# Kernel tuning notes

Measured on AMD Instinct MI355X. Metric: run time of the kernel, lower is better.

The kernel has to match this reference:

```python
import jax, jax.numpy as jnp
import numpy as np

THETA = 0.7
KS = 3          # deformable-conv kernel size
N = KS * KS     # 9 sampling points


def setup_inputs() -> dict:
    key = jax.random.key(0)
    k = jax.random.split(key, 7)
    B, C, H, W = 2, 256, 64, 64
    x = jax.random.normal(k[0], (B, C, H, W), jnp.float32)
    # offset-predicting conv (3x3, pad 1), 2*N output channels; small init so offsets are sane
    p_w = jax.random.normal(k[1], (2 * N, C, 3, 3), jnp.float32) * 0.01
    p_b = jax.random.normal(k[2], (2 * N,), jnp.float32) * 0.01
    # modulation conv (3x3, pad 1), N output channels
    m_w = jax.random.normal(k[3], (N, C, 3, 3), jnp.float32) * 0.01
    m_b = jnp.zeros((N,), jnp.float32)
    # final deform conv weight (applied as ks x ks, stride ks over the unfolded map), no bias
    dconv_w = jax.random.normal(k[4], (256, C, KS, KS), jnp.float32) * 0.05
    # central-difference conv raw weight, shape (Cout, Cin, 1, 5), no bias
    cdc_w = jax.random.normal(k[5], (256, C, 1, 5), jnp.float32) * 0.05
    return {"x": x, "p_w": p_w, "p_b": p_b, "m_w": m_w, "m_b": m_b,
            "dconv_w": dconv_w, "cdc_w": cdc_w}


def _conv2d(x, w, pad):
    return jax.lax.conv_general_dilated(
        x, w, window_strides=(1, 1), padding=pad,
        dimension_numbers=("NCHW", "OIHW", "NCHW"))


def deform_conv(x, p_w, p_b, m_w, m_b, dconv_w):
    B, C, H, W = x.shape
    same = [(1, 1), (1, 1)]
    offset = _conv2d(x, p_w, same) + p_b[None, :, None, None]          # [B,2N,H,W]
    m = jax.nn.sigmoid(_conv2d(x, m_w, same) + m_b[None, :, None, None])  # [B,N,H,W]

    xp = jnp.pad(x, ((0, 0), (0, 0), (1, 1), (1, 1)))  # zero padding 1
    Hp, Wp = H + 2, W + 2

    # p = p_0 + p_n + offset  (x = row coord, y = col coord; torch meshgrid 'ij')
    p_n_x = jnp.repeat(jnp.arange(-1, 2, dtype=x.dtype), 3)   # [-1,-1,-1,0,0,0,1,1,1]
    p_n_y = jnp.tile(jnp.arange(-1, 2, dtype=x.dtype), 3)     # [-1,0,1,-1,0,1,-1,0,1]
    rows = jnp.arange(1, H + 1, dtype=x.dtype)                # p_0_x
    cols = jnp.arange(1, W + 1, dtype=x.dtype)                # p_0_y
    px = offset[:, :N] + p_n_x[None, :, None, None] + rows[None, None, :, None]
    py = offset[:, N:] + p_n_y[None, :, None, None] + cols[None, None, None, :]
    px = jnp.transpose(px, (0, 2, 3, 1))  # [B,H,W,N]
    py = jnp.transpose(py, (0, 2, 3, 1))

    # integer corners from UNCLAMPED p (detached), as in the original
    fx = jnp.floor(jax.lax.stop_gradient(px))
    fy = jnp.floor(jax.lax.stop_gradient(py))
    qx0 = jnp.clip(fx, 0, Hp - 1)
    qy0 = jnp.clip(fy, 0, Wp - 1)
    qx1 = jnp.clip(fx + 1, 0, Hp - 1)
    qy1 = jnp.clip(fy + 1, 0, Wp - 1)

    # clamp p before computing bilinear weights (original order)
    pxc = jnp.clip(px, 0, Hp - 1)
    pyc = jnp.clip(py, 0, Wp - 1)
    g_lt = (1 + (qx0 - pxc)) * (1 + (qy0 - pyc))
    g_rb = (1 - (qx1 - pxc)) * (1 - (qy1 - pyc))
    g_lb = (1 + (qx0 - pxc)) * (1 - (qy1 - pyc))
    g_rt = (1 - (qx1 - pxc)) * (1 + (qy0 - pyc))

    xf = xp.reshape(B, C, Hp * Wp)

    def gather(qx, qy):
        idx = (qx.astype(jnp.int32) * Wp + qy.astype(jnp.int32)).reshape(B, 1, -1)
        return jnp.take_along_axis(xf, idx, axis=2).reshape(B, C, H, W, N)

    x_off = (g_lt[:, None] * gather(qx0, qy0)
             + g_rb[:, None] * gather(qx1, qy1)
             + g_lb[:, None] * gather(qx0, qy1)
             + g_rt[:, None] * gather(qx1, qy0))          # [B,C,H,W,N]
    x_off = x_off * jnp.transpose(m, (0, 2, 3, 1))[:, None]  # modulation broadcast over C

    # conv(ksxks, stride ks) over the unfolded map == contraction over the N taps;
    # tap n = 3r + c corresponds to kernel position (r, c)
    w = dconv_w.reshape(dconv_w.shape[0], C, N)
    return jnp.einsum("bchwn,ocn->bohw", x_off, w)


def cdc_conv(x, cdc_w):
    Co, Ci = cdc_w.shape[0], cdc_w.shape[1]
    z = jnp.zeros((Co, Ci, 1), cdc_w.dtype)
    wk = jnp.concatenate(
        [z, cdc_w[:, :, :, 0], z, cdc_w[:, :, :, 1], cdc_w[:, :, :, 2],
         cdc_w[:, :, :, 3], z, cdc_w[:, :, :, 4], z], axis=2
    ).reshape(Co, Ci, 3, 3)
    out_normal = _conv2d(x, wk, [(1, 1), (1, 1)])
    kdiff = cdc_w.sum(axis=(2, 3))[:, :, None, None]
    out_diff = _conv2d(x, kdiff, [(0, 0), (0, 0)])
    return out_normal - THETA * out_diff


def reference(x, p_w, p_b, m_w, m_b, dconv_w, cdc_w):
    out_dc = jax.nn.relu(deform_conv(x, p_w, p_b, m_w, m_b, dconv_w))
    out_cdc = jax.nn.relu(cdc_conv(x, cdc_w))
    return jnp.concatenate([out_dc, out_cdc], axis=1)  # [B,512,H,W]
```

## Files before the change

kernel.cpp:

```cpp
#include <hip/hip_runtime.h>
#include <hip/hip_bf16.h>
#include <math.h>

#define XT_BSTRIDE (66*66*256)
#define THETA_ 0.7f

typedef unsigned short u16;
typedef __attribute__((ext_vector_type(8))) short bf16x8;
typedef __attribute__((ext_vector_type(4))) float f32x4;

#define GLOAD16(gp, lp) __builtin_amdgcn_global_load_lds( \
    (const __attribute__((address_space(1))) unsigned int*)(gp), \
    (__attribute__((address_space(3))) unsigned int*)(lp), 16, 0, 0)

#define WAIT_VMCNT(N) asm volatile("s_waitcnt vmcnt(" #N ")" ::: "memory")

__device__ __forceinline__ void bar_fenced() {
  __builtin_amdgcn_sched_barrier(0);
  __builtin_amdgcn_s_barrier();
  __builtin_amdgcn_sched_barrier(0);
}

__device__ __forceinline__ float bf2f(u16 v) {
  union { unsigned u; float f; } x; x.u = ((unsigned)v) << 16; return x.f;
}
__device__ __forceinline__ u16 f2bf(float f) {
  __hip_bfloat16 h = __float2bfloat16(f);
  return *(u16*)&h;
}

__device__ __forceinline__ size_t swz_idx(int row, int k, int KT) {
  int kt = k >> 6, kc = (k >> 3) & 7, kj = k & 7;
  return (size_t)row * KT + kt * 64 + ((kc ^ (row & 7)) << 3) + kj;
}

__global__ __launch_bounds__(256) void prep(
    const float* __restrict__ x, const float* __restrict__ p_w,
    const float* __restrict__ m_w, const float* __restrict__ dconv_w,
    const float* __restrict__ cdc_w, u16* __restrict__ xTb,
    u16* __restrict__ W1t, u16* __restrict__ Wdt, u16* __restrict__ Wct) {
  int blk = blockIdx.x;
  if (blk < 512) {
    int cg = blk & 3;
    int h  = (blk >> 2) & 63;
    int b  = blk >> 8;
    __shared__ float tile[64][65];
    const float* xp = x + ((size_t)(b * 256 + cg * 64)) * 4096 + h * 64;
#pragma unroll
    for (int j = 0; j < 16; j++) {
      int idx = j * 256 + threadIdx.x;
      int ci = idx >> 6, w = idx & 63;
      tile[ci][w] = xp[(size_t)ci * 4096 + w];
    }
    __syncthreads();
    u16* xo = xTb + (size_t)b * XT_BSTRIDE + ((h + 1) * 66 + 1) * 256 + cg * 64;
#pragma unroll
    for (int j = 0; j < 16; j++) {
      int idx = j * 256 + threadIdx.x;
      int w = idx >> 6, ci = idx & 63;
      xo[(size_t)w * 256 + ci] = f2bf(tile[ci][w]);
    }
    return;
  }
  if (blk < 1032) {
    int i = (blk - 512) * 256 + threadIdx.x;
    if (i >= 133120) return;
    int c = i & 255;
    int j = i >> 8;
    int b = (j >= 260) ? 1 : 0;
    int r = j - b * 260;
    int hp, wp;
    if (r < 66)       { hp = 0;        wp = r; }
    else if (r < 132) { hp = 65;       wp = r - 66; }
    else if (r < 196) { hp = r - 131;  wp = 0; }
    else              { hp = r - 195;  wp = 65; }
    xTb[(size_t)b * XT_BSTRIDE + (hp * 66 + wp) * 256 + c] = 0;
    return;
  }
  int i = (blk - 1032) * 256 + threadIdx.x;
  if (i < 73728) {
    int o = i / 2304, k = i % 2304;
    int kp = k >> 8, c = k & 255;
    float v = 0.f;
    if (o < 18)      v = p_w[((size_t)o * 256 + c) * 9 + kp];
    else if (o < 27) v = m_w[((size_t)(o - 18) * 256 + c) * 9 + kp];
    W1t[swz_idx(o, k, 2304)] = f2bf(v);
    return;
  }
  int j = i - 73728;
  if (j < 589824) {
    int o = j / 2304, k = j % 2304;
    int n = k >> 8, c = k & 255;
    Wdt[swz_idx(o, k, 2304)] = f2bf(dconv_w[((size_t)o * 256 + c) * 9 + n]);
    return;
  }
  int j2 = j - 589824;
  if (j2 < 327680) {
    int o = j2 / 1280, k = j2 % 1280;
    int t = k >> 8, c = k & 255;
    const float* cw = cdc_w + ((size_t)o * 256 + c) * 5;
    float v = cw[t];
    if (t == 2) v -= THETA_ * (cw[0] + cw[1] + cw[2] + cw[3] + cw[4]);
    Wct[swz_idx(o, k, 1280)] = f2bf(v);
  }
}

__global__ __launch_bounds__(256) void gather_Ad(const u16* __restrict__ xTb,
                                                 const float* __restrict__ omp,
                                                 const float* __restrict__ p_b,
                                                 const float* __restrict__ m_b,
                                                 u16* __restrict__ Ad) {
  int gid = blockIdx.x * 256 + threadIdx.x;
  int q = gid & 31;
  int s = gid >> 5;
  int p = s / 9, n = s - p * 9;
  int b = p >> 12;
  int hw = p & 4095;
  int h = hw >> 6, w = hw & 63;

  float offx = p_b[n], offy = p_b[9 + n], mraw = m_b[n];
#pragma unroll
  for (int ks = 0; ks < 4; ks++) {
    const float* base = omp + ks * 221184 + b * 110592;
    offx += base[(size_t)n * 4096 + hw];
    offy += base[(size_t)(9 + n) * 4096 + hw];
    mraw += base[(size_t)(18 + n) * 4096 + hw];
  }
  float px = offx + (float)(h + n / 3);
  float py = offy + (float)(w + n % 3);
  float fx = floorf(px), fy = floorf(py);
  float qx0 = fminf(fmaxf(fx, 0.f), 65.f);
  float qy0 = fminf(fmaxf(fy, 0.f), 65.f);
  float qx1 = fminf(fmaxf(fx + 1.f, 0.f), 65.f);
  float qy1 = fminf(fmaxf(fy + 1.f, 0.f), 65.f);
  float pxc = fminf(fmaxf(px, 0.f), 65.f);
  float pyc = fminf(fmaxf(py, 0.f), 65.f);
  float gx0 = 1.f + (qx0 - pxc);
  float gx1 = 1.f - (qx1 - pxc);
  float gy0 = 1.f + (qy0 - pyc);
  float gy1 = 1.f - (qy1 - pyc);
  float m = 1.f / (1.f + expf(-mraw));
  int i0 = (int)qx0 * 66 + (int)qy0;
  int i1 = (int)qx1 * 66 + (int)qy1;
  int i2 = (int)qx0 * 66 + (int)qy1;
  int i3 = (int)qx1 * 66 + (int)qy0;
  float g0 = gx0 * gy0 * m, g1 = gx1 * gy1 * m;
  float g2 = gx0 * gy1 * m, g3 = gx1 * gy0 * m;

  const u16* xb = xTb + (size_t)b * XT_BSTRIDE + q * 8;
  bf16x8 a0 = *(const bf16x8*)(xb + (size_t)i0 * 256);
  bf16x8 a1 = *(const bf16x8*)(xb + (size_t)i1 * 256);
  bf16x8 a2 = *(const bf16x8*)(xb + (size_t)i2 * 256);
  bf16x8 a3 = *(const bf16x8*)(xb + (size_t)i3 * 256);
  bf16x8 ov;
#pragma unroll
  for (int j = 0; j < 8; j++) {
    float v = g0 * bf2f((u16)a0[j]) + g1 * bf2f((u16)a1[j]) +
              g2 * bf2f((u16)a2[j]) + g3 * bf2f((u16)a3[j]);
    ov[j] = (short)f2bf(v);
  }
  int k = n * 256 + q * 8;
  int kt = k >> 6, kc = (k >> 3) & 7;
  *(bf16x8*)(Ad + (size_t)p * 2304 + kt * 64 + (((kc ^ (p & 7)) << 3))) = ov;
}

template <int KTOT, int MODE>
__device__ __forceinline__ void gemm_body(
    const u16* __restrict__ Asrc, const u16* __restrict__ Bt,
    float* __restrict__ outp, int mt, int nt, u16* As, u16* Bs) {
  const int NKT = KTOT / 64;
  const int OCH0 = (MODE == 1) ? 256 : 0;
  int tid = threadIdx.x;
  int wid = tid >> 6, lane = tid & 63;
  int wr = wid >> 1, wc = wid & 1;
  int pbase = mt * 64;
  int obase = nt * 64;
  int l8 = lane >> 3, l7 = lane & 7;
  int lr = lane & 15, lg = lane >> 4;

  f32x4 acc[2][2];
#pragma unroll
  for (int i = 0; i < 2; i++)
#pragma unroll
    for (int j = 0; j < 2; j++) acc[i][j] = {0.f, 0.f, 0.f, 0.f};

  const int dh1[5] = {0, 1, 1, 1, 2}, dw1[5] = {1, 0, 1, 2, 1};

  auto stage = [&](int kt, u16* Ah, u16* Bh) {
    if (MODE == 0) {
#pragma unroll
      for (int i = 0; i < 2; i++) {
        int r0 = wid * 16 + i * 8;
        const u16* g = Asrc + (size_t)(pbase + r0 + l8) * KTOT + kt * 64 + (l7 << 3);
        GLOAD16(g, &Ah[r0 * 64]);
      }
    } else {
      int t = kt >> 2, c0 = (kt & 3) << 6;
      int dh = dh1[t], dw = dw1[t];
#pragma unroll
      for (int i = 0; i < 2; i++) {
        int r0 = wid * 16 + i * 8;
        int r = r0 + l8;
        int p = pbase + r;
        int b = p >> 12, hw = p & 4095, h = hw >> 6, w = hw & 63;
        int chunk = l7 ^ (r & 7);
        const u16* g = Asrc + (size_t)b * XT_BSTRIDE +
                       ((h + dh) * 66 + (w + dw)) * 256 + c0 + (chunk << 3);
        GLOAD16(g, &Ah[r0 * 64]);
      }
    }
#pragma unroll
    for (int i = 0; i < 2; i++) {
      int o0 = wid * 16 + i * 8;
      const u16* g = Bt + (size_t)(obase + o0 + l8) * KTOT + kt * 64 + (l7 << 3);
      GLOAD16(g, &Bh[o0 * 64]);
    }
  };

  stage(0, As, Bs);

  for (int it = 0; it < NKT; it++) {
    int cur = it & 1;
    u16* Ac = As + cur * 4096;
    u16* Bc = Bs + cur * 4096;

    bar_fenced();
    if (it + 1 < NKT) {
      stage(it + 1, As + (cur ^ 1) * 4096, Bs + (cur ^ 1) * 4096);
      WAIT_VMCNT(4);
    } else {
      WAIT_VMCNT(0);
    }
    bar_fenced();

    bf16x8 av[2][2], bv[2][2];
#pragma unroll
    for (int mf = 0; mf < 2; mf++) {
      int r = wr * 32 + mf * 16 + lr;
#pragma unroll
      for (int ks = 0; ks < 2; ks++) {
        int kc = ks * 4 + lg;
        av[mf][ks] = *(const bf16x8*)&Ac[r * 64 + ((kc ^ (r & 7)) << 3)];
      }
    }
#pragma unroll
    for (int nf = 0; nf < 2; nf++) {
      int o = wc * 32 + nf * 16 + lr;
#pragma unroll
      for (int ks = 0; ks < 2; ks++) {
        int kc = ks * 4 + lg;
        bv[nf][ks] = *(const bf16x8*)&Bc[o * 64 + ((kc ^ (o & 7)) << 3)];
      }
    }
#pragma unroll
    for (int nf = 0; nf < 2; nf++)
#pragma unroll
      for (int mf = 0; mf < 2; mf++)
#pragma unroll
        for (int ks = 0; ks < 2; ks++)
          acc[nf][mf] = __builtin_amdgcn_mfma_f32_16x16x32_bf16(
              bv[nf][ks], av[mf][ks], acc[nf][mf], 0, 0, 0);
  }

#pragma unroll
  for (int nf = 0; nf < 2; nf++)
#pragma unroll
    for (int mf = 0; mf < 2; mf++) {
      int p = pbase + wr * 32 + mf * 16 + lr;
      int hw = p & 4095, b = p >> 12;
      int og = OCH0 + obase + wc * 32 + nf * 16 + lg * 4;
      f32x4 v = acc[nf][mf];
#pragma unroll
      for (int e = 0; e < 4; e++)
        outp[(size_t)(b * 512 + og + e) * 4096 + hw] = fmaxf(v[e], 0.f);
    }
}

__device__ __forceinline__ void offmod_body(
    const u16* __restrict__ xTb, const u16* __restrict__ Bt,
    float* __restrict__ outp, int mt, int kt0, int nkt, u16* As, u16* Bs) {
  int tid = threadIdx.x;
  int wid = tid >> 6, lane = tid & 63;
  int pbase = mt * 128;
  int l8 = lane >> 3, l7 = lane & 7;
  int lr = lane & 15, lg = lane >> 4;

  f32x4 acc[2][2];
#pragma unroll
  for (int i = 0; i < 2; i++)
#pragma unroll
    for (int j = 0; j < 2; j++) acc[i][j] = {0.f, 0.f, 0.f, 0.f};

  auto stage = [&](int kt, u16* Ah, u16* Bh) {
    int t = kt >> 2, c0 = (kt & 3) << 6;
    int dh = t / 3, dw = t % 3;
#pragma unroll
    for (int i = 0; i < 4; i++) {
      int r0 = wid * 32 + i * 8;
      int r = r0 + l8;
      int p = pbase + r;
      int b = p >> 12, hw = p & 4095, h = hw >> 6, w = hw & 63;
      int chunk = l7 ^ (r & 7);
      const u16* g = xTb + (size_t)b * XT_BSTRIDE +
                     ((h + dh) * 66 + (w + dw)) * 256 + c0 + (chunk << 3);
      GLOAD16(g, &Ah[r0 * 64]);
    }
    {
      int o0 = wid * 8;
      const u16* g = Bt + (size_t)(o0 + l8) * 2304 + kt * 64 + (l7 << 3);
      GLOAD16(g, &Bh[o0 * 64]);
    }
  };

  stage(kt0, As, Bs);

  for (int it = 0; it < nkt; it++) {
    int cur = it & 1;
    u16* Ac = As + cur * 8192;
    u16* Bc = Bs + cur * 2048;

    bar_fenced();
    if (it + 1 < nkt) {
      stage(kt0 + it + 1, As + (cur ^ 1) * 8192, Bs + (cur ^ 1) * 2048);
      WAIT_VMCNT(5);
    } else {
      WAIT_VMCNT(0);
    }
    bar_fenced();

    bf16x8 av[2][2], bv[2][2];
#pragma unroll
    for (int mf = 0; mf < 2; mf++) {
      int r = wid * 32 + mf * 16 + lr;
#pragma unroll
      for (int ks = 0; ks < 2; ks++) {
        int kc = ks * 4 + lg;
        av[mf][ks] = *(const bf16x8*)&Ac[r * 64 + ((kc ^ (r & 7)) << 3)];
      }
    }
#pragma unroll
    for (int nf = 0; nf < 2; nf++) {
      int o = nf * 16 + lr;
#pragma unroll
      for (int ks = 0; ks < 2; ks++) {
        int kc = ks * 4 + lg;
        bv[nf][ks] = *(const bf16x8*)&Bc[o * 64 + ((kc ^ (o & 7)) << 3)];
      }
    }
#pragma unroll
    for (int nf = 0; nf < 2; nf++)
#pragma unroll
      for (int mf = 0; mf < 2; mf++)
#pragma unroll
        for (int ks = 0; ks < 2; ks++)
          acc[nf][mf] = __builtin_amdgcn_mfma_f32_16x16x32_bf16(
              bv[nf][ks], av[mf][ks], acc[nf][mf], 0, 0, 0);
  }

#pragma unroll
  for (int nf = 0; nf < 2; nf++)
#pragma unroll
    for (int mf = 0; mf < 2; mf++) {
      int p = pbase + wid * 32 + mf * 16 + lr;
      int hw = p & 4095, b = p >> 12;
      int o0 = nf * 16 + lg * 4;
      f32x4 v = acc[nf][mf];
#pragma unroll
      for (int e = 0; e < 4; e++) {
        int o = o0 + e;
        if (o < 27)
          outp[(size_t)(b * 27 + o) * 4096 + hw] = v[e];
      }
    }
}

__global__ __launch_bounds__(256) void gemm_offmod(const u16* __restrict__ xTb,
                                                   const u16* __restrict__ W1t,
                                                   float* __restrict__ omp) {
  __shared__ u16 As[2 * 128 * 64];
  __shared__ u16 Bs[2 * 32 * 64];
  int bid = blockIdx.x;
  int xcd = bid & 7;
  int i = bid >> 3;
  int mt = xcd * 8 + (i & 7);
  int ks = i >> 3;
  offmod_body(xTb, W1t, omp + ks * 221184, mt, ks * 9, 9, As, Bs);
}

__global__ __launch_bounds__(256, 4) void gemm_main(const u16* __restrict__ Ad,
                                                    const u16* __restrict__ xTb,
                                                    const u16* __restrict__ Wdt,
                                                    const u16* __restrict__ Wct,
                                                    float* __restrict__ out) {
  __shared__ u16 As[2 * 64 * 64];
  __shared__ u16 Bs[2 * 64 * 64];
  int bid = blockIdx.x;
  int fam = bid & 1;
  int idx = bid >> 1;
  int xcd = idx & 7;
  int j = idx >> 3;
  int mt = xcd * 16 + (j & 15);
  int nt = j >> 4;
  if (fam == 0) gemm_body<2304, 0>(Ad, Wdt, out, mt, nt, As, Bs);
  else          gemm_body<1280, 1>(xTb, Wct, out, mt, nt, As, Bs);
}

extern "C" void kernel_launch(void* const* d_in, const int* in_sizes, int n_in,
                              void* d_out, int out_size, void* d_ws, size_t ws_size,
                              hipStream_t stream) {
  (void)in_sizes; (void)n_in; (void)out_size; (void)ws_size;
  const float* x       = (const float*)d_in[0];
  const float* p_w     = (const float*)d_in[1];
  const float* p_b     = (const float*)d_in[2];
  const float* m_w     = (const float*)d_in[3];
  const float* m_b     = (const float*)d_in[4];
  const float* dconv_w = (const float*)d_in[5];
  const float* cdc_w   = (const float*)d_in[6];
  float* out = (float*)d_out;
  char* ws = (char*)d_ws;

  u16*   xTb  = (u16*)(ws);
  float* omp  = (float*)(ws + 4460544);
  u16*   W1t  = (u16*)(ws + 7999488);
  u16*   Wdt  = (u16*)(ws + 8146944);
  u16*   Wct  = (u16*)(ws + 9326592);
  u16*   Ad   = (u16*)(ws + 9981952);

  prep<<<4904, 256, 0, stream>>>(x, p_w, m_w, dconv_w, cdc_w, xTb, W1t, Wdt, Wct);
  gemm_offmod<<<256, 256, 0, stream>>>(xTb, W1t, omp);
  gather_Ad<<<9216, 256, 0, stream>>>(xTb, omp, p_b, m_b, Ad);
  gemm_main<<<1024, 256, 0, stream>>>(Ad, xTb, Wdt, Wct, out);
}
```

Measured before the change: 63.03 us.

## Fuse deformable bilinear gather into the main GEMM kernel per block

Removes the separate gather_Ad launch. Each deform block now computes its own sampling indices and weights into shared memory, gathers its 64-row A tile into a private global scratch slice, then runs the GEMM on it. The deform GEMM tile widens to 64x128 output channels and the CDC GEMM moves into its own specialised body. Each 64-row A tile is now gathered twice, once per output-channel half, and the scratch footprint doubles. The aim is to save a launch and keep the freshly gathered A tile hot in L2.

After: 70.88 us. 12.5% more time.

```diff
diff --git a/kernel.cpp b/kernel.cpp
--- a/kernel.cpp
+++ b/kernel.cpp
@@ -105,177 +105,6 @@
   }
 }
 
-__global__ __launch_bounds__(256) void gather_Ad(const u16* __restrict__ xTb,
-                                                 const float* __restrict__ omp,
-                                                 const float* __restrict__ p_b,
-                                                 const float* __restrict__ m_b,
-                                                 u16* __restrict__ Ad) {
-  int gid = blockIdx.x * 256 + threadIdx.x;
-  int q = gid & 31;
-  int s = gid >> 5;
-  int p = s / 9, n = s - p * 9;
-  int b = p >> 12;
-  int hw = p & 4095;
-  int h = hw >> 6, w = hw & 63;
-
-  float offx = p_b[n], offy = p_b[9 + n], mraw = m_b[n];
-#pragma unroll
-  for (int ks = 0; ks < 4; ks++) {
-    const float* base = omp + ks * 221184 + b * 110592;
-    offx += base[(size_t)n * 4096 + hw];
-    offy += base[(size_t)(9 + n) * 4096 + hw];
-    mraw += base[(size_t)(18 + n) * 4096 + hw];
-  }
-  float px = offx + (float)(h + n / 3);
-  float py = offy + (float)(w + n % 3);
-  float fx = floorf(px), fy = floorf(py);
-  float qx0 = fminf(fmaxf(fx, 0.f), 65.f);
-  float qy0 = fminf(fmaxf(fy, 0.f), 65.f);
-  float qx1 = fminf(fmaxf(fx + 1.f, 0.f), 65.f);
-  float qy1 = fminf(fmaxf(fy + 1.f, 0.f), 65.f);
-  float pxc = fminf(fmaxf(px, 0.f), 65.f);
-  float pyc = fminf(fmaxf(py, 0.f), 65.f);
-  float gx0 = 1.f + (qx0 - pxc);
-  float gx1 = 1.f - (qx1 - pxc);
-  float gy0 = 1.f + (qy0 - pyc);
-  float gy1 = 1.f - (qy1 - pyc);
-  float m = 1.f / (1.f + expf(-mraw));
-  int i0 = (int)qx0 * 66 + (int)qy0;
-  int i1 = (int)qx1 * 66 + (int)qy1;
-  int i2 = (int)qx0 * 66 + (int)qy1;
-  int i3 = (int)qx1 * 66 + (int)qy0;
-  float g0 = gx0 * gy0 * m, g1 = gx1 * gy1 * m;
-  float g2 = gx0 * gy1 * m, g3 = gx1 * gy0 * m;
-
-  const u16* xb = xTb + (size_t)b * XT_BSTRIDE + q * 8;
-  bf16x8 a0 = *(const bf16x8*)(xb + (size_t)i0 * 256);
-  bf16x8 a1 = *(const bf16x8*)(xb + (size_t)i1 * 256);
-  bf16x8 a2 = *(const bf16x8*)(xb + (size_t)i2 * 256);
-  bf16x8 a3 = *(const bf16x8*)(xb + (size_t)i3 * 256);
-  bf16x8 ov;
-#pragma unroll
-  for (int j = 0; j < 8; j++) {
-    float v = g0 * bf2f((u16)a0[j]) + g1 * bf2f((u16)a1[j]) +
-              g2 * bf2f((u16)a2[j]) + g3 * bf2f((u16)a3[j]);
-    ov[j] = (short)f2bf(v);
-  }
-  int k = n * 256 + q * 8;
-  int kt = k >> 6, kc = (k >> 3) & 7;
-  *(bf16x8*)(Ad + (size_t)p * 2304 + kt * 64 + (((kc ^ (p & 7)) << 3))) = ov;
-}
-
-template <int KTOT, int MODE>
-__device__ __forceinline__ void gemm_body(
-    const u16* __restrict__ Asrc, const u16* __restrict__ Bt,
-    float* __restrict__ outp, int mt, int nt, u16* As, u16* Bs) {
-  const int NKT = KTOT / 64;
-  const int OCH0 = (MODE == 1) ? 256 : 0;
-  int tid = threadIdx.x;
-  int wid = tid >> 6, lane = tid & 63;
-  int wr = wid >> 1, wc = wid & 1;
-  int pbase = mt * 64;
-  int obase = nt * 64;
-  int l8 = lane >> 3, l7 = lane & 7;
-  int lr = lane & 15, lg = lane >> 4;
-
-  f32x4 acc[2][2];
-#pragma unroll
-  for (int i = 0; i < 2; i++)
-#pragma unroll
-    for (int j = 0; j < 2; j++) acc[i][j] = {0.f, 0.f, 0.f, 0.f};
-
-  const int dh1[5] = {0, 1, 1, 1, 2}, dw1[5] = {1, 0, 1, 2, 1};
-
-  auto stage = [&](int kt, u16* Ah, u16* Bh) {
-    if (MODE == 0) {
-#pragma unroll
-      for (int i = 0; i < 2; i++) {
-        int r0 = wid * 16 + i * 8;
-        const u16* g = Asrc + (size_t)(pbase + r0 + l8) * KTOT + kt * 64 + (l7 << 3);
-        GLOAD16(g, &Ah[r0 * 64]);
-      }
-    } else {
-      int t = kt >> 2, c0 = (kt & 3) << 6;
-      int dh = dh1[t], dw = dw1[t];
-#pragma unroll
-      for (int i = 0; i < 2; i++) {
-        int r0 = wid * 16 + i * 8;
-        int r = r0 + l8;
-        int p = pbase + r;
-        int b = p >> 12, hw = p & 4095, h = hw >> 6, w = hw & 63;
-        int chunk = l7 ^ (r & 7);
-        const u16* g = Asrc + (size_t)b * XT_BSTRIDE +
-                       ((h + dh) * 66 + (w + dw)) * 256 + c0 + (chunk << 3);
-        GLOAD16(g, &Ah[r0 * 64]);
-      }
-    }
-#pragma unroll
-    for (int i = 0; i < 2; i++) {
-      int o0 = wid * 16 + i * 8;
-      const u16* g = Bt + (size_t)(obase + o0 + l8) * KTOT + kt * 64 + (l7 << 3);
-      GLOAD16(g, &Bh[o0 * 64]);
-    }
-  };
-
-  stage(0, As, Bs);
-
-  for (int it = 0; it < NKT; it++) {
-    int cur = it & 1;
-    u16* Ac = As + cur * 4096;
-    u16* Bc = Bs + cur * 4096;
-
-    bar_fenced();
-    if (it + 1 < NKT) {
-      stage(it + 1, As + (cur ^ 1) * 4096, Bs + (cur ^ 1) * 4096);
-      WAIT_VMCNT(4);
-    } else {
-      WAIT_VMCNT(0);
-    }
-    bar_fenced();
-
-    bf16x8 av[2][2], bv[2][2];
-#pragma unroll
-    for (int mf = 0; mf < 2; mf++) {
-      int r = wr * 32 + mf * 16 + lr;
-#pragma unroll
-      for (int ks = 0; ks < 2; ks++) {
-        int kc = ks * 4 + lg;
-        av[mf][ks] = *(const bf16x8*)&Ac[r * 64 + ((kc ^ (r & 7)) << 3)];
-      }
-    }
-#pragma unroll
-    for (int nf = 0; nf < 2; nf++) {
-      int o = wc * 32 + nf * 16 + lr;
-#pragma unroll
-      for (int ks = 0; ks < 2; ks++) {
-        int kc = ks * 4 + lg;
-        bv[nf][ks] = *(const bf16x8*)&Bc[o * 64 + ((kc ^ (o & 7)) << 3)];
-      }
-    }
-#pragma unroll
-    for (int nf = 0; nf < 2; nf++)
-#pragma unroll
-      for (int mf = 0; mf < 2; mf++)
-#pragma unroll
-        for (int ks = 0; ks < 2; ks++)
-          acc[nf][mf] = __builtin_amdgcn_mfma_f32_16x16x32_bf16(
-              bv[nf][ks], av[mf][ks], acc[nf][mf], 0, 0, 0);
-  }
-
-#pragma unroll
-  for (int nf = 0; nf < 2; nf++)
-#pragma unroll
-    for (int mf = 0; mf < 2; mf++) {
-      int p = pbase + wr * 32 + mf * 16 + lr;
-      int hw = p & 4095, b = p >> 12;
-      int og = OCH0 + obase + wc * 32 + nf * 16 + lg * 4;
-      f32x4 v = acc[nf][mf];
-#pragma unroll
-      for (int e = 0; e < 4; e++)
-        outp[(size_t)(b * 512 + og + e) * 4096 + hw] = fmaxf(v[e], 0.f);
-    }
-}
-
 __device__ __forceinline__ void offmod_body(
     const u16* __restrict__ xTb, const u16* __restrict__ Bt,
     float* __restrict__ outp, int mt, int kt0, int nkt, u16* As, u16* Bs) {
@@ -387,22 +216,296 @@
   offmod_body(xTb, W1t, omp + ks * 221184, mt, ks * 9, 9, As, Bs);
 }
 
-__global__ __launch_bounds__(256, 4) void gemm_main(const u16* __restrict__ Ad,
-                                                    const u16* __restrict__ xTb,
-                                                    const u16* __restrict__ Wdt,
-                                                    const u16* __restrict__ Wct,
-                                                    float* __restrict__ out) {
-  __shared__ u16 As[2 * 64 * 64];
-  __shared__ u16 Bs[2 * 64 * 64];
+__device__ void cdc_body(const u16* __restrict__ xTb, const u16* __restrict__ Bt,
+                         float* __restrict__ outp, int mt, int nt,
+                         u16* As, u16* Bs) {
+  const int NKT = 20;
+  int tid = threadIdx.x;
+  int wid = tid >> 6, lane = tid & 63;
+  int wr = wid >> 1, wc = wid & 1;
+  int pbase = mt * 64;
+  int obase = nt * 64;
+  int l8 = lane >> 3, l7 = lane & 7;
+  int lr = lane & 15, lg = lane >> 4;
+
+  f32x4 acc[2][2];
+#pragma unroll
+  for (int i = 0; i < 2; i++)
+#pragma unroll
+    for (int j = 0; j < 2; j++) acc[i][j] = {0.f, 0.f, 0.f, 0.f};
+
+  const int dh1[5] = {0, 1, 1, 1, 2}, dw1[5] = {1, 0, 1, 2, 1};
+
+  auto stage = [&](int kt, u16* Ah, u16* Bh) {
+    int t = kt >> 2, c0 = (kt & 3) << 6;
+    int dh = dh1[t], dw = dw1[t];
+#pragma unroll
+    for (int i = 0; i < 2; i++) {
+      int r0 = wid * 16 + i * 8;
+      int r = r0 + l8;
+      int p = pbase + r;
+      int b = p >> 12, hw = p & 4095, h = hw >> 6, w = hw & 63;
+      int chunk = l7 ^ (r & 7);
+      const u16* g = xTb + (size_t)b * XT_BSTRIDE +
+                     ((h + dh) * 66 + (w + dw)) * 256 + c0 + (chunk << 3);
+      GLOAD16(g, &Ah[r0 * 64]);
+    }
+#pragma unroll
+    for (int i = 0; i < 2; i++) {
+      int o0 = wid * 16 + i * 8;
+      const u16* g = Bt + (size_t)(obase + o0 + l8) * 1280 + kt * 64 + (l7 << 3);
+      GLOAD16(g, &Bh[o0 * 64]);
+    }
+  };
+
+  stage(0, As, Bs);
+
+  for (int it = 0; it < NKT; it++) {
+    int cur = it & 1;
+    u16* Ac = As + cur * 4096;
+    u16* Bc = Bs + cur * 4096;
+
+    bar_fenced();
+    if (it + 1 < NKT) {
+      stage(it + 1, As + (cur ^ 1) * 4096, Bs + (cur ^ 1) * 4096);
+      WAIT_VMCNT(4);
+    } else {
+      WAIT_VMCNT(0);
+    }
+    bar_fenced();
+
+    bf16x8 av[2][2], bv[2][2];
+#pragma unroll
+    for (int mf = 0; mf < 2; mf++) {
+      int r = wr * 32 + mf * 16 + lr;
+#pragma unroll
+      for (int ks = 0; ks < 2; ks++) {
+        int kc = ks * 4 + lg;
+        av[mf][ks] = *(const bf16x8*)&Ac[r * 64 + ((kc ^ (r & 7)) << 3)];
+      }
+    }
+#pragma unroll
+    for (int nf = 0; nf < 2; nf++) {
+      int o = wc * 32 + nf * 16 + lr;
+#pragma unroll
+      for (int ks = 0; ks < 2; ks++) {
+        int kc = ks * 4 + lg;
+        bv[nf][ks] = *(const bf16x8*)&Bc[o * 64 + ((kc ^ (o & 7)) << 3)];
+      }
+    }
+#pragma unroll
+    for (int nf = 0; nf < 2; nf++)
+#pragma unroll
+      for (int mf = 0; mf < 2; mf++)
+#pragma unroll
+        for (int ks = 0; ks < 2; ks++)
+          acc[nf][mf] = __builtin_amdgcn_mfma_f32_16x16x32_bf16(
+              bv[nf][ks], av[mf][ks], acc[nf][mf], 0, 0, 0);
+  }
+
+#pragma unroll
+  for (int nf = 0; nf < 2; nf++)
+#pragma unroll
+    for (int mf = 0; mf < 2; mf++) {
+      int p = pbase + wr * 32 + mf * 16 + lr;
+      int hw = p & 4095, b = p >> 12;
+      int og = 256 + obase + wc * 32 + nf * 16 + lg * 4;
+      f32x4 v = acc[nf][mf];
+#pragma unroll
+      for (int e = 0; e < 4; e++)
+        outp[(size_t)(b * 512 + og + e) * 4096 + hw] = fmaxf(v[e], 0.f);
+    }
+}
+
+__device__ void deform_body(const u16* __restrict__ xTb,
+                            const float* __restrict__ omp,
+                            const float* __restrict__ p_b,
+                            const float* __restrict__ m_b,
+                            const u16* __restrict__ Wdt,
+                            u16* __restrict__ Adp,
+                            float* __restrict__ out, int mt, int nt, u16* S) {
+  const int NKT = 36;
+  int tid = threadIdx.x;
+  int wid = tid >> 6, lane = tid & 63;
+  int wr = wid >> 1, wc = wid & 1;
+  int l8 = lane >> 3, l7 = lane & 7;
+  int lr = lane & 15, lg = lane >> 4;
+  int pbase = mt * 64;
+  int obase = nt * 128;
+  int b = pbase >> 12;
+  const u16* xb = xTb + (size_t)b * XT_BSTRIDE;
+
+  int4* Sidx = (int4*)S;
+  float4* Sg = (float4*)(S + 4608);
+#pragma unroll
+  for (int r = 0; r < 3; r++) {
+    int sl = r * 256 + tid;
+    if (sl < 576) {
+      int pl = sl / 9;
+      int n = sl - pl * 9;
+      int p = pbase + pl;
+      int hw = p & 4095;
+      int h = hw >> 6, w = hw & 63;
+      float offx = p_b[n], offy = p_b[9 + n], mraw = m_b[n];
+#pragma unroll
+      for (int ks = 0; ks < 4; ks++) {
+        const float* base = omp + ks * 221184 + b * 110592;
+        offx += base[(size_t)n * 4096 + hw];
+        offy += base[(size_t)(9 + n) * 4096 + hw];
+        mraw += base[(size_t)(18 + n) * 4096 + hw];
+      }
+      float px = offx + (float)(h + n / 3);
+      float py = offy + (float)(w + n % 3);
+      float fx = floorf(px), fy = floorf(py);
+      float qx0 = fminf(fmaxf(fx, 0.f), 65.f);
+      float qy0 = fminf(fmaxf(fy, 0.f), 65.f);
+      float qx1 = fminf(fmaxf(fx + 1.f, 0.f), 65.f);
+      float qy1 = fminf(fmaxf(fy + 1.f, 0.f), 65.f);
+      float pxc = fminf(fmaxf(px, 0.f), 65.f);
+      float pyc = fminf(fmaxf(py, 0.f), 65.f);
+      float gx0 = 1.f + (qx0 - pxc);
+      float gx1 = 1.f - (qx1 - pxc);
+      float gy0 = 1.f + (qy0 - pyc);
+      float gy1 = 1.f - (qy1 - pyc);
+      float m = 1.f / (1.f + expf(-mraw));
+      Sidx[sl] = make_int4((int)qx0 * 66 + (int)qy0, (int)qx1 * 66 + (int)qy1,
+                           (int)qx0 * 66 + (int)qy1, (int)qx1 * 66 + (int)qy0);
+      Sg[sl] = make_float4(gx0 * gy0 * m, gx1 * gy1 * m,
+                           gx0 * gy1 * m, gx1 * gy0 * m);
+    }
+  }
+  __syncthreads();
+
+#pragma unroll 4
+  for (int it2 = 0; it2 < 72; it2++) {
+    int task = it2 * 256 + tid;
+    int sl = task >> 5, q = task & 31;
+    int4 qi = Sidx[sl];
+    float4 g = Sg[sl];
+    int pl = sl / 9, n = sl - pl * 9;
+    const u16* xc = xb + q * 8;
+    bf16x8 a0 = *(const bf16x8*)(xc + (size_t)qi.x * 256);
+    bf16x8 a1 = *(const bf16x8*)(xc + (size_t)qi.y * 256);
+    bf16x8 a2 = *(const bf16x8*)(xc + (size_t)qi.z * 256);
+    bf16x8 a3 = *(const bf16x8*)(xc + (size_t)qi.w * 256);
+    bf16x8 ov;
+#pragma unroll
+    for (int j = 0; j < 8; j++) {
+      float v = g.x * bf2f((u16)a0[j]) + g.y * bf2f((u16)a1[j]) +
+                g.z * bf2f((u16)a2[j]) + g.w * bf2f((u16)a3[j]);
+      ov[j] = (short)f2bf(v);
+    }
+    int k = n * 256 + q * 8;
+    int kt = k >> 6, kc = (k >> 3) & 7;
+    *(bf16x8*)&Adp[(size_t)pl * 2304 + kt * 64 + ((kc ^ (pl & 7)) << 3)] = ov;
+  }
+  __syncthreads();
+
+  f32x4 acc[4][2];
+#pragma unroll
+  for (int i = 0; i < 4; i++)
+#pragma unroll
+    for (int j = 0; j < 2; j++) acc[i][j] = {0.f, 0.f, 0.f, 0.f};
+
+  u16* A0 = S;
+  u16* B0 = S + 8192;
+
+  auto stage = [&](int kt, u16* Ah, u16* Bh) {
+#pragma unroll
+    for (int i = 0; i < 2; i++) {
+      int r0 = wid * 16 + i * 8;
+      const u16* g = Adp + (size_t)(r0 + l8) * 2304 + kt * 64 + (l7 << 3);
+      GLOAD16(g, &Ah[r0 * 64]);
+    }
+#pragma unroll
+    for (int i = 0; i < 4; i++) {
+      int o0 = wid * 32 + i * 8;
+      const u16* g = Wdt + (size_t)(obase + o0 + l8) * 2304 + kt * 64 + (l7 << 3);
+      GLOAD16(g, &Bh[o0 * 64]);
+    }
+  };
+
+  stage(0, A0, B0);
+
+  for (int it = 0; it < NKT; it++) {
+    int cur = it & 1;
+    u16* Ac = A0 + cur * 4096;
+    u16* Bc = B0 + cur * 8192;
+
+    bar_fenced();
+    if (it + 1 < NKT) {
+      stage(it + 1, A0 + (cur ^ 1) * 4096, B0 + (cur ^ 1) * 8192);
+      WAIT_VMCNT(6);
+    } else {
+      WAIT_VMCNT(0);
+    }
+    bar_fenced();
+
+    bf16x8 av[2][2], bv[4][2];
+#pragma unroll
+    for (int mf = 0; mf < 2; mf++) {
+      int r = wr * 32 + mf * 16 + lr;
+#pragma unroll
+      for (int ks = 0; ks < 2; ks++) {
+        int kc = ks * 4 + lg;
+        av[mf][ks] = *(const bf16x8*)&Ac[r * 64 + ((kc ^ (r & 7)) << 3)];
+      }
+    }
+#pragma unroll
+    for (int nf = 0; nf < 4; nf++) {
+      int o = wc * 64 + nf * 16 + lr;
+#pragma unroll
+      for (int ks = 0; ks < 2; ks++) {
+        int kc = ks * 4 + lg;
+        bv[nf][ks] = *(const bf16x8*)&Bc[o * 64 + ((kc ^ (o & 7)) << 3)];
+      }
+    }
+#pragma unroll
+    for (int nf = 0; nf < 4; nf++)
+#pragma unroll
+      for (int mf = 0; mf < 2; mf++)
+#pragma unroll
+        for (int ks = 0; ks < 2; ks++)
+          acc[nf][mf] = __builtin_amdgcn_mfma_f32_16x16x32_bf16(
+              bv[nf][ks], av[mf][ks], acc[nf][mf], 0, 0, 0);
+  }
+
+#pragma unroll
+  for (int nf = 0; nf < 4; nf++)
+#pragma unroll
+    for (int mf = 0; mf < 2; mf++) {
+      int p = pbase + wr * 32 + mf * 16 + lr;
+      int hw = p & 4095;
+      int og = obase + wc * 64 + nf * 16 + lg * 4;
+      f32x4 v = acc[nf][mf];
+#pragma unroll
+      for (int e = 0; e < 4; e++)
+        out[(size_t)(b * 512 + og + e) * 4096 + hw] = fmaxf(v[e], 0.f);
+    }
+}
+
+__global__ __launch_bounds__(256, 3) void gemm_main(
+    const u16* __restrict__ xTb, const float* __restrict__ omp,
+    const float* __restrict__ p_b, const float* __restrict__ m_b,
+    const u16* __restrict__ Wdt, const u16* __restrict__ Wct,
+    u16* __restrict__ Ad, float* __restrict__ out) {
+  __shared__ u16 S[24576];
   int bid = blockIdx.x;
-  int fam = bid & 1;
-  int idx = bid >> 1;
-  int xcd = idx & 7;
-  int j = idx >> 3;
-  int mt = xcd * 16 + (j & 15);
-  int nt = j >> 4;
-  if (fam == 0) gemm_body<2304, 0>(Ad, Wdt, out, mt, nt, As, Bs);
-  else          gemm_body<1280, 1>(xTb, Wct, out, mt, nt, As, Bs);
+  if (bid < 256) {
+    int xcd = bid & 7;
+    int j = bid >> 3;
+    int mt = xcd * 16 + (j & 15);
+    int nt = j >> 4;
+    u16* Adp = Ad + (size_t)bid * (64 * 2304);
+    deform_body(xTb, omp, p_b, m_b, Wdt, Adp, out, mt, nt, S);
+  } else {
+    int b2 = bid - 256;
+    int xcd = b2 & 7;
+    int j = b2 >> 3;
+    int mt = xcd * 16 + (j & 15);
+    int nt = j >> 4;
+    cdc_body(xTb, Wct, out, mt, nt, S, S + 8192);
+  }
 }
 
 extern "C" void kernel_launch(void* const* d_in, const int* in_sizes, int n_in,
@@ -428,6 +531,5 @@
 
   prep<<<4904, 256, 0, stream>>>(x, p_w, m_w, dconv_w, cdc_w, xTb, W1t, Wdt, Wct);
   gemm_offmod<<<256, 256, 0, stream>>>(xTb, W1t, omp);
-  gather_Ad<<<9216, 256, 0, stream>>>(xTb, omp, p_b, m_b, Ad);
-  gemm_main<<<1024, 256, 0, stream>>>(Ad, xTb, Wdt, Wct, out);
-}
+  gemm_main<<<768, 256, 0, stream>>>(xTb, omp, p_b, m_b, Wdt, Wct, Ad, out);
+}
```

## Move CDC GEMM blocks into the gather kernel to overlap with deform gather

Applied to the files above, without the earlier changes.

The central-difference-conv GEMM tiles move out of the main GEMM kernel into the gather kernel. The first 512 blocks of that launch run the CDC GEMM and the remaining blocks do the deformable bilinear gather. The aim is to overlap the independent CDC matmul with the memory-bound gather and shrink the final GEMM launch to only the deform branch. In exchange, the gather launch now carries a 32KB static LDS allocation for every block, which may reduce occupancy for the gather blocks.

Measured after the change: 67.55 us. 7.2% more time.

```diff
diff --git a/kernel.cpp b/kernel.cpp
--- a/kernel.cpp
+++ b/kernel.cpp
@@ -105,12 +105,245 @@
   }
 }
 
-__global__ __launch_bounds__(256) void gather_Ad(const u16* __restrict__ xTb,
-                                                 const float* __restrict__ omp,
-                                                 const float* __restrict__ p_b,
-                                                 const float* __restrict__ m_b,
-                                                 u16* __restrict__ Ad) {
-  int gid = blockIdx.x * 256 + threadIdx.x;
+template <int KTOT, int MODE>
+__device__ __forceinline__ void gemm_body(
+    const u16* __restrict__ Asrc, const u16* __restrict__ Bt,
+    float* __restrict__ outp, int mt, int nt, u16* As, u16* Bs) {
+  const int NKT = KTOT / 64;
+  const int OCH0 = (MODE == 1) ? 256 : 0;
+  int tid = threadIdx.x;
+  int wid = tid >> 6, lane = tid & 63;
+  int wr = wid >> 1, wc = wid & 1;
+  int pbase = mt * 64;
+  int obase = nt * 64;
+  int l8 = lane >> 3, l7 = lane & 7;
+  int lr = lane & 15, lg = lane >> 4;
+
+  f32x4 acc[2][2];
+#pragma unroll
+  for (int i = 0; i < 2; i++)
+#pragma unroll
+    for (int j = 0; j < 2; j++) acc[i][j] = {0.f, 0.f, 0.f, 0.f};
+
+  const int dh1[5] = {0, 1, 1, 1, 2}, dw1[5] = {1, 0, 1, 2, 1};
+
+  auto stage = [&](int kt, u16* Ah, u16* Bh) {
+    if (MODE == 0) {
+#pragma unroll
+      for (int i = 0; i < 2; i++) {
+        int r0 = wid * 16 + i * 8;
+        const u16* g = Asrc + (size_t)(pbase + r0 + l8) * KTOT + kt * 64 + (l7 << 3);
+        GLOAD16(g, &Ah[r0 * 64]);
+      }
+    } else {
+      int t = kt >> 2, c0 = (kt & 3) << 6;
+      int dh = dh1[t], dw = dw1[t];
+#pragma unroll
+      for (int i = 0; i < 2; i++) {
+        int r0 = wid * 16 + i * 8;
+        int r = r0 + l8;
+        int p = pbase + r;
+        int b = p >> 12, hw = p & 4095, h = hw >> 6, w = hw & 63;
+        int chunk = l7 ^ (r & 7);
+        const u16* g = Asrc + (size_t)b * XT_BSTRIDE +
+                       ((h + dh) * 66 + (w + dw)) * 256 + c0 + (chunk << 3);
+        GLOAD16(g, &Ah[r0 * 64]);
+      }
+    }
+#pragma unroll
+    for (int i = 0; i < 2; i++) {
+      int o0 = wid * 16 + i * 8;
+      const u16* g = Bt + (size_t)(obase + o0 + l8) * KTOT + kt * 64 + (l7 << 3);
+      GLOAD16(g, &Bh[o0 * 64]);
+    }
+  };
+
+  stage(0, As, Bs);
+
+  for (int it = 0; it < NKT; it++) {
+    int cur = it & 1;
+    u16* Ac = As + cur * 4096;
+    u16* Bc = Bs + cur * 4096;
+
+    bar_fenced();
+    if (it + 1 < NKT) {
+      stage(it + 1, As + (cur ^ 1) * 4096, Bs + (cur ^ 1) * 4096);
+      WAIT_VMCNT(4);
+    } else {
+      WAIT_VMCNT(0);
+    }
+    bar_fenced();
+
+    bf16x8 av[2][2], bv[2][2];
+#pragma unroll
+    for (int mf = 0; mf < 2; mf++) {
+      int r = wr * 32 + mf * 16 + lr;
+#pragma unroll
+      for (int ks = 0; ks < 2; ks++) {
+        int kc = ks * 4 + lg;
+        av[mf][ks] = *(const bf16x8*)&Ac[r * 64 + ((kc ^ (r & 7)) << 3)];
+      }
+    }
+#pragma unroll
+    for (int nf = 0; nf < 2; nf++) {
+      int o = wc * 32 + nf * 16 + lr;
+#pragma unroll
+      for (int ks = 0; ks < 2; ks++) {
+        int kc = ks * 4 + lg;
+        bv[nf][ks] = *(const bf16x8*)&Bc[o * 64 + ((kc ^ (o & 7)) << 3)];
+      }
+    }
+#pragma unroll
+    for (int nf = 0; nf < 2; nf++)
+#pragma unroll
+      for (int mf = 0; mf < 2; mf++)
+#pragma unroll
+        for (int ks = 0; ks < 2; ks++)
+          acc[nf][mf] = __builtin_amdgcn_mfma_f32_16x16x32_bf16(
+              bv[nf][ks], av[mf][ks], acc[nf][mf], 0, 0, 0);
+  }
+
+#pragma unroll
+  for (int nf = 0; nf < 2; nf++)
+#pragma unroll
+    for (int mf = 0; mf < 2; mf++) {
+      int p = pbase + wr * 32 + mf * 16 + lr;
+      int hw = p & 4095, b = p >> 12;
+      int og = OCH0 + obase + wc * 32 + nf * 16 + lg * 4;
+      f32x4 v = acc[nf][mf];
+#pragma unroll
+      for (int e = 0; e < 4; e++)
+        outp[(size_t)(b * 512 + og + e) * 4096 + hw] = fmaxf(v[e], 0.f);
+    }
+}
+
+__device__ __forceinline__ void offmod_body(
+    const u16* __restrict__ xTb, const u16* __restrict__ Bt,
+    float* __restrict__ outp, int mt, int kt0, int nkt, u16* As, u16* Bs) {
+  int tid = threadIdx.x;
+  int wid = tid >> 6, lane = tid & 63;
+  int pbase = mt * 128;
+  int l8 = lane >> 3, l7 = lane & 7;
+  int lr = lane & 15, lg = lane >> 4;
+
+  f32x4 acc[2][2];
+#pragma unroll
+  for (int i = 0; i < 2; i++)
+#pragma unroll
+    for (int j = 0; j < 2; j++) acc[i][j] = {0.f, 0.f, 0.f, 0.f};
+
+  auto stage = [&](int kt, u16* Ah, u16* Bh) {
+    int t = kt >> 2, c0 = (kt & 3) << 6;
+    int dh = t / 3, dw = t % 3;
+#pragma unroll
+    for (int i = 0; i < 4; i++) {
+      int r0 = wid * 32 + i * 8;
+      int r = r0 + l8;
+      int p = pbase + r;
+      int b = p >> 12, hw = p & 4095, h = hw >> 6, w = hw & 63;
+      int chunk = l7 ^ (r & 7);
+      const u16* g = xTb + (size_t)b * XT_BSTRIDE +
+                     ((h + dh) * 66 + (w + dw)) * 256 + c0 + (chunk << 3);
+      GLOAD16(g, &Ah[r0 * 64]);
+    }
+    {
+      int o0 = wid * 8;
+      const u16* g = Bt + (size_t)(o0 + l8) * 2304 + kt * 64 + (l7 << 3);
+      GLOAD16(g, &Bh[o0 * 64]);
+    }
+  };
+
+  stage(kt0, As, Bs);
+
+  for (int it = 0; it < nkt; it++) {
+    int cur = it & 1;
+    u16* Ac = As + cur * 8192;
+    u16* Bc = Bs + cur * 2048;
+
+    bar_fenced();
+    if (it + 1 < nkt) {
+      stage(kt0 + it + 1, As + (cur ^ 1) * 8192, Bs + (cur ^ 1) * 2048);
+      WAIT_VMCNT(5);
+    } else {
+      WAIT_VMCNT(0);
+    }
+    bar_fenced();
+
+    bf16x8 av[2][2], bv[2][2];
+#pragma unroll
+    for (int mf = 0; mf < 2; mf++) {
+      int r = wid * 32 + mf * 16 + lr;
+#pragma unroll
+      for (int ks = 0; ks < 2; ks++) {
+        int kc = ks * 4 + lg;
+        av[mf][ks] = *(const bf16x8*)&Ac[r * 64 + ((kc ^ (r & 7)) << 3)];
+      }
+    }
+#pragma unroll
+    for (int nf = 0; nf < 2; nf++) {
+      int o = nf * 16 + lr;
+#pragma unroll
+      for (int ks = 0; ks < 2; ks++) {
+        int kc = ks * 4 + lg;
+        bv[nf][ks] = *(const bf16x8*)&Bc[o * 64 + ((kc ^ (o & 7)) << 3)];
+      }
+    }
+#pragma unroll
+    for (int nf = 0; nf < 2; nf++)
+#pragma unroll
+      for (int mf = 0; mf < 2; mf++)
+#pragma unroll
+        for (int ks = 0; ks < 2; ks++)
+          acc[nf][mf] = __builtin_amdgcn_mfma_f32_16x16x32_bf16(
+              bv[nf][ks], av[mf][ks], acc[nf][mf], 0, 0, 0);
+  }
+
+#pragma unroll
+  for (int nf = 0; nf < 2; nf++)
+#pragma unroll
+    for (int mf = 0; mf < 2; mf++) {
+      int p = pbase + wid * 32 + mf * 16 + lr;
+      int hw = p & 4095, b = p >> 12;
+      int o0 = nf * 16 + lg * 4;
+      f32x4 v = acc[nf][mf];
+#pragma unroll
+      for (int e = 0; e < 4; e++) {
+        int o = o0 + e;
+        if (o < 27)
+          outp[(size_t)(b * 27 + o) * 4096 + hw] = v[e];
+      }
+    }
+}
+
+__global__ __launch_bounds__(256) void gemm_offmod(const u16* __restrict__ xTb,
+                                                   const u16* __restrict__ W1t,
+                                                   float* __restrict__ omp) {
+  __shared__ u16 As[2 * 128 * 64];
+  __shared__ u16 Bs[2 * 32 * 64];
+  int bid = blockIdx.x;
+  int xcd = bid & 7;
+  int i = bid >> 3;
+  int mt = xcd * 8 + (i & 7);
+  int ks = i >> 3;
+  offmod_body(xTb, W1t, omp + ks * 221184, mt, ks * 9, 9, As, Bs);
+}
+
+__global__ __launch_bounds__(256) void gather_cdc(
+    const u16* __restrict__ xTb, const float* __restrict__ omp,
+    const float* __restrict__ p_b, const float* __restrict__ m_b,
+    const u16* __restrict__ Wct, u16* __restrict__ Ad,
+    float* __restrict__ out) {
+  __shared__ u16 S[16384];
+  int bid = blockIdx.x;
+  if (bid < 512) {
+    int xcd = bid & 7;
+    int j = bid >> 3;
+    int mt = xcd * 16 + (j & 15);
+    int nt = j >> 4;
+    gemm_body<1280, 1>(xTb, Wct, out, mt, nt, S, S + 8192);
+    return;
+  }
+  int gid = (bid - 512) * 256 + threadIdx.x;
   int q = gid & 31;
   int s = gid >> 5;
   int p = s / 9, n = s - p * 9;
@@ -164,245 +397,17 @@
   *(bf16x8*)(Ad + (size_t)p * 2304 + kt * 64 + (((kc ^ (p & 7)) << 3))) = ov;
 }
 
-template <int KTOT, int MODE>
-__device__ __forceinline__ void gemm_body(
-    const u16* __restrict__ Asrc, const u16* __restrict__ Bt,
-    float* __restrict__ outp, int mt, int nt, u16* As, u16* Bs) {
-  const int NKT = KTOT / 64;
-  const int OCH0 = (MODE == 1) ? 256 : 0;
-  int tid = threadIdx.x;
-  int wid = tid >> 6, lane = tid & 63;
-  int wr = wid >> 1, wc = wid & 1;
-  int pbase = mt * 64;
-  int obase = nt * 64;
-  int l8 = lane >> 3, l7 = lane & 7;
-  int lr = lane & 15, lg = lane >> 4;
-
-  f32x4 acc[2][2];
-#pragma unroll
-  for (int i = 0; i < 2; i++)
-#pragma unroll
-    for (int j = 0; j < 2; j++) acc[i][j] = {0.f, 0.f, 0.f, 0.f};
-
-  const int dh1[5] = {0, 1, 1, 1, 2}, dw1[5] = {1, 0, 1, 2, 1};
-
-  auto stage = [&](int kt, u16* Ah, u16* Bh) {
-    if (MODE == 0) {
-#pragma unroll
-      for (int i = 0; i < 2; i++) {
-        int r0 = wid * 16 + i * 8;
-        const u16* g = Asrc + (size_t)(pbase + r0 + l8) * KTOT + kt * 64 + (l7 << 3);
-        GLOAD16(g, &Ah[r0 * 64]);
-      }
-    } else {
-      int t = kt >> 2, c0 = (kt & 3) << 6;
-      int dh = dh1[t], dw = dw1[t];
-#pragma unroll
-      for (int i = 0; i < 2; i++) {
-        int r0 = wid * 16 + i * 8;
-        int r = r0 + l8;
-        int p = pbase + r;
-        int b = p >> 12, hw = p & 4095, h = hw >> 6, w = hw & 63;
-        int chunk = l7 ^ (r & 7);
-        const u16* g = Asrc + (size_t)b * XT_BSTRIDE +
-                       ((h + dh) * 66 + (w + dw)) * 256 + c0 + (chunk << 3);
-        GLOAD16(g, &Ah[r0 * 64]);
-      }
-    }
-#pragma unroll
-    for (int i = 0; i < 2; i++) {
-      int o0 = wid * 16 + i * 8;
-      const u16* g = Bt + (size_t)(obase + o0 + l8) * KTOT + kt * 64 + (l7 << 3);
-      GLOAD16(g, &Bh[o0 * 64]);
-    }
-  };
-
-  stage(0, As, Bs);
-
-  for (int it = 0; it < NKT; it++) {
-    int cur = it & 1;
-    u16* Ac = As + cur * 4096;
-    u16* Bc = Bs + cur * 4096;
-
-    bar_fenced();
-    if (it + 1 < NKT) {
-      stage(it + 1, As + (cur ^ 1) * 4096, Bs + (cur ^ 1) * 4096);
-      WAIT_VMCNT(4);
-    } else {
-      WAIT_VMCNT(0);
-    }
-    bar_fenced();
-
-    bf16x8 av[2][2], bv[2][2];
-#pragma unroll
-    for (int mf = 0; mf < 2; mf++) {
-      int r = wr * 32 + mf * 16 + lr;
-#pragma unroll
-      for (int ks = 0; ks < 2; ks++) {
-        int kc = ks * 4 + lg;
-        av[mf][ks] = *(const bf16x8*)&Ac[r * 64 + ((kc ^ (r & 7)) << 3)];
-      }
-    }
-#pragma unroll
-    for (int nf = 0; nf < 2; nf++) {
-      int o = wc * 32 + nf * 16 + lr;
-#pragma unroll
-      for (int ks = 0; ks < 2; ks++) {
-        int kc = ks * 4 + lg;
-        bv[nf][ks] = *(const bf16x8*)&Bc[o * 64 + ((kc ^ (o & 7)) << 3)];
-      }
-    }
-#pragma unroll
-    for (int nf = 0; nf < 2; nf++)
-#pragma unroll
-      for (int mf = 0; mf < 2; mf++)
-#pragma unroll
-        for (int ks = 0; ks < 2; ks++)
-          acc[nf][mf] = __builtin_amdgcn_mfma_f32_16x16x32_bf16(
-              bv[nf][ks], av[mf][ks], acc[nf][mf], 0, 0, 0);
-  }
-
-#pragma unroll
-  for (int nf = 0; nf < 2; nf++)
-#pragma unroll
-    for (int mf = 0; mf < 2; mf++) {
-      int p = pbase + wr * 32 + mf * 16 + lr;
-      int hw = p & 4095, b = p >> 12;
-      int og = OCH0 + obase + wc * 32 + nf * 16 + lg * 4;
-      f32x4 v = acc[nf][mf];
-#pragma unroll
-      for (int e = 0; e < 4; e++)
-        outp[(size_t)(b * 512 + og + e) * 4096 + hw] = fmaxf(v[e], 0.f);
-    }
-}
-
-__device__ __forceinline__ void offmod_body(
-    const u16* __restrict__ xTb, const u16* __restrict__ Bt,
-    float* __restrict__ outp, int mt, int kt0, int nkt, u16* As, u16* Bs) {
-  int tid = threadIdx.x;
-  int wid = tid >> 6, lane = tid & 63;
-  int pbase = mt * 128;
-  int l8 = lane >> 3, l7 = lane & 7;
-  int lr = lane & 15, lg = lane >> 4;
-
-  f32x4 acc[2][2];
-#pragma unroll
-  for (int i = 0; i < 2; i++)
-#pragma unroll
-    for (int j = 0; j < 2; j++) acc[i][j] = {0.f, 0.f, 0.f, 0.f};
-
-  auto stage = [&](int kt, u16* Ah, u16* Bh) {
-    int t = kt >> 2, c0 = (kt & 3) << 6;
-    int dh = t / 3, dw = t % 3;
-#pragma unroll
-    for (int i = 0; i < 4; i++) {
-      int r0 = wid * 32 + i * 8;
-      int r = r0 + l8;
-      int p = pbase + r;
-      int b = p >> 12, hw = p & 4095, h = hw >> 6, w = hw & 63;
-      int chunk = l7 ^ (r & 7);
-      const u16* g = xTb + (size_t)b * XT_BSTRIDE +
-                     ((h + dh) * 66 + (w + dw)) * 256 + c0 + (chunk << 3);
-      GLOAD16(g, &Ah[r0 * 64]);
-    }
-    {
-      int o0 = wid * 8;
-      const u16* g = Bt + (size_t)(o0 + l8) * 2304 + kt * 64 + (l7 << 3);
-      GLOAD16(g, &Bh[o0 * 64]);
-    }
-  };
-
-  stage(kt0, As, Bs);
-
-  for (int it = 0; it < nkt; it++) {
-    int cur = it & 1;
-    u16* Ac = As + cur * 8192;
-    u16* Bc = Bs + cur * 2048;
-
-    bar_fenced();
-    if (it + 1 < nkt) {
-      stage(kt0 + it + 1, As + (cur ^ 1) * 8192, Bs + (cur ^ 1) * 2048);
-      WAIT_VMCNT(5);
-    } else {
-      WAIT_VMCNT(0);
-    }
-    bar_fenced();
-
-    bf16x8 av[2][2], bv[2][2];
-#pragma unroll
-    for (int mf = 0; mf < 2; mf++) {
-      int r = wid * 32 + mf * 16 + lr;
-#pragma unroll
-      for (int ks = 0; ks < 2; ks++) {
-        int kc = ks * 4 + lg;
-        av[mf][ks] = *(const bf16x8*)&Ac[r * 64 + ((kc ^ (r & 7)) << 3)];
-      }
-    }
-#pragma unroll
-    for (int nf = 0; nf < 2; nf++) {
-      int o = nf * 16 + lr;
-#pragma unroll
-      for (int ks = 0; ks < 2; ks++) {
-        int kc = ks * 4 + lg;
-        bv[nf][ks] = *(const bf16x8*)&Bc[o * 64 + ((kc ^ (o & 7)) << 3)];
-      }
-    }
-#pragma unroll
-    for (int nf = 0; nf < 2; nf++)
-#pragma unroll
-      for (int mf = 0; mf < 2; mf++)
-#pragma unroll
-        for (int ks = 0; ks < 2; ks++)
-          acc[nf][mf] = __builtin_amdgcn_mfma_f32_16x16x32_bf16(
-              bv[nf][ks], av[mf][ks], acc[nf][mf], 0, 0, 0);
-  }
-
-#pragma unroll
-  for (int nf = 0; nf < 2; nf++)
-#pragma unroll
-    for (int mf = 0; mf < 2; mf++) {
-      int p = pbase + wid * 32 + mf * 16 + lr;
-      int hw = p & 4095, b = p >> 12;
-      int o0 = nf * 16 + lg * 4;
-      f32x4 v = acc[nf][mf];
-#pragma unroll
-      for (int e = 0; e < 4; e++) {
-        int o = o0 + e;
-        if (o < 27)
-          outp[(size_t)(b * 27 + o) * 4096 + hw] = v[e];
-      }
-    }
-}
-
-__global__ __launch_bounds__(256) void gemm_offmod(const u16* __restrict__ xTb,
-                                                   const u16* __restrict__ W1t,
-                                                   float* __restrict__ omp) {
-  __shared__ u16 As[2 * 128 * 64];
-  __shared__ u16 Bs[2 * 32 * 64];
-  int bid = blockIdx.x;
-  int xcd = bid & 7;
-  int i = bid >> 3;
-  int mt = xcd * 8 + (i & 7);
-  int ks = i >> 3;
-  offmod_body(xTb, W1t, omp + ks * 221184, mt, ks * 9, 9, As, Bs);
-}
-
 __global__ __launch_bounds__(256, 4) void gemm_main(const u16* __restrict__ Ad,
-                                                    const u16* __restrict__ xTb,
                                                     const u16* __restrict__ Wdt,
-                                                    const u16* __restrict__ Wct,
                                                     float* __restrict__ out) {
   __shared__ u16 As[2 * 64 * 64];
   __shared__ u16 Bs[2 * 64 * 64];
   int bid = blockIdx.x;
-  int fam = bid & 1;
-  int idx = bid >> 1;
-  int xcd = idx & 7;
-  int j = idx >> 3;
+  int xcd = bid & 7;
+  int j = bid >> 3;
   int mt = xcd * 16 + (j & 15);
   int nt = j >> 4;
-  if (fam == 0) gemm_body<2304, 0>(Ad, Wdt, out, mt, nt, As, Bs);
-  else          gemm_body<1280, 1>(xTb, Wct, out, mt, nt, As, Bs);
+  gemm_body<2304, 0>(Ad, Wdt, out, mt, nt, As, Bs);
 }
 
 extern "C" void kernel_launch(void* const* d_in, const int* in_sizes, int n_in,
@@ -428,6 +433,6 @@
 
   prep<<<4904, 256, 0, stream>>>(x, p_w, m_w, dconv_w, cdc_w, xTb, W1t, Wdt, Wct);
   gemm_offmod<<<256, 256, 0, stream>>>(xTb, W1t, omp);
-  gather_Ad<<<9216, 256, 0, stream>>>(xTb, omp, p_b, m_b, Ad);
-  gemm_main<<<1024, 256, 0, stream>>>(Ad, xTb, Wdt, Wct, out);
-}
+  gather_cdc<<<9728, 256, 0, stream>>>(xTb, omp, p_b, m_b, Wct, Ad, out);
+  gemm_main<<<512, 256, 0, stream>>>(Ad, Wdt, out);
+}
```
